# Kernel optimization log

Hardware: AMD Instinct MI355X
Metric: run time of the kernel (lower is better)

## Reference

```python
import jax, jax.numpy as jnp
import numpy as np

B, C, H, W, D = 4, 8, 160, 160, 160
N_PER = 100000
IMAGE_DIM = 160


def setup_inputs() -> dict:
    key = jax.random.key(0)
    k1, k2 = jax.random.split(key)
    image_features = jax.random.normal(k1, (B, C, H, W, D), dtype=jnp.float32)
    # coords uniform in [0, IMAGE_DIM); last 3 columns are x,y,z
    graph_features = jax.random.uniform(k2, (B * N_PER, 3), dtype=jnp.float32) * IMAGE_DIM
    batch = jnp.arange(B * N_PER, dtype=jnp.int32) // N_PER  # equal count per image (required by cat dim=0)
    return {
        "image_features": image_features,
        "graph_features": graph_features,
        "batch": batch,
        "image_dim": IMAGE_DIM,
    }


def _trilerp(image_features, graph_features, image_dim):
    Bn, Cc, Hh, Ww, Dd = image_features.shape
    n_per = graph_features.shape[0] // Bn
    dt = graph_features.dtype
    factor = jnp.asarray(image_dim, dt) / Hh  # original uses image_dim/h for all axes
    xyz = graph_features[:, -3:].reshape(Bn, n_per, 3) / factor  # [B, n, 3]
    x, y, z = xyz[..., 0], xyz[..., 1], xyz[..., 2]

    def bounds(v, size):
        lo = jnp.minimum(jnp.floor(v), size - 1)
        hi = jnp.minimum(jnp.ceil(v), size - 1)
        return lo, hi

    x1f, x2f = bounds(x, Hh)
    y1f, y2f = bounds(y, Ww)
    z1f, z2f = bounds(z, Dd)
    x1, x2 = x1f.astype(jnp.int32), x2f.astype(jnp.int32)
    y1, y2 = y1f.astype(jnp.int32), y2f.astype(jnp.int32)
    z1, z2 = z1f.astype(jnp.int32), z2f.astype(jnp.int32)
    # weights exactly as in original (degenerate-to-zero when floor==ceil, kept faithfully)
    wx, wx2 = x - x1f, x2f - x
    wy, wy2 = y - y1f, y2f - y
    wz, wz2 = z - z1f, z2f - z

    def per_image(img, x1, x2, y1, y2, z1, z2, wx, wx2, wy, wy2, wz, wz2):
        # img: [C, H, W, D]; indices/weights: [n]
        def g(xi, yi, zi):
            return img[:, xi, yi, zi]  # [C, n]

        def lerp_y(zc):
            lx1 = g(x2, y1, zc) * wx + g(x1, y1, zc) * wx2
            lx2 = g(x2, y2, zc) * wx + g(x1, y2, zc) * wx2
            return lx2 * wy + lx1 * wy2

        return lerp_y(z2) * wz + lerp_y(z1) * wz2  # [C, n]

    out = jax.vmap(per_image)(
        image_features, x1, x2, y1, y2, z1, z2, wx, wx2, wy, wy2, wz, wz2
    )  # [B, C, n]
    # torch.cat over batch along dim 0 of [C, n] blocks == reshape to [B*C, n]; then permute(1,0)
    return out.reshape(Bn * Cc, n_per).T  # [n, B*C]


def reference(image_features, graph_features, batch, image_dim):
    # batch is arange(N)//n_per (sorted, equal counts), so grouping == reshape; batch unused numerically
    return _trilerp(image_features, graph_features, image_dim)
```

## Files before the change

### kernel.cpp

```cpp
#include <hip/hip_runtime.h>

constexpr int B = 4, C = 8, H = 160, W = 160, Dd = 160, NPER = 100000;
constexpr long HWD = (long)H * W * Dd;
constexpr int  TOTAL_PTS = NPER * B;
constexpr int  TOTAL_OUT = NPER * B * C;
constexpr int  NKEYS = B * H * W;
constexpr int  SCAN_BLOCKS = NKEYS / 256;

typedef float f32x4 __attribute__((ext_vector_type(4)));

constexpr size_t WS_COUNTS_OFF = 0;
constexpr size_t WS_PART_OFF   = (size_t)NKEYS * 4;
constexpr size_t WS_PAY_OFF    = WS_PART_OFF + 4096;
constexpr size_t WS_NEEDED     = WS_PAY_OFF + (size_t)TOTAL_PTS * 16;

__device__ __forceinline__ float load_image_dim(const int* dimp) {
    int iv = dimp[0];
    return (iv > 0 && iv < 1000000) ? (float)iv : __int_as_float(iv);
}

struct Coord {
    int x1, x2, y1, y2, z1, z2;
    float wx, wx2, wy, wy2, wz, wz2;
};
__device__ __forceinline__ Coord coord_from_xyz(float gx, float gy, float gz,
                                                float factor) {
    Coord c;
    float x = gx / factor, y = gy / factor, z = gz / factor;
    float x1f = fminf(floorf(x), (float)(H - 1));
    float x2f = fminf(ceilf(x),  (float)(H - 1));
    float y1f = fminf(floorf(y), (float)(W - 1));
    float y2f = fminf(ceilf(y),  (float)(W - 1));
    float z1f = fminf(floorf(z), (float)(Dd - 1));
    float z2f = fminf(ceilf(z),  (float)(Dd - 1));
    c.x1 = max(0, (int)x1f); c.x2 = max(0, (int)x2f);
    c.y1 = max(0, (int)y1f); c.y2 = max(0, (int)y2f);
    c.z1 = max(0, (int)z1f); c.z2 = max(0, (int)z2f);
    c.wx = x - x1f; c.wx2 = x2f - x;
    c.wy = y - y1f; c.wy2 = y2f - y;
    c.wz = z - z1f; c.wz2 = z2f - z;
    return c;
}

__global__ __launch_bounds__(256) void zero_kernel(int* __restrict__ counts) {
    int i = blockIdx.x * 256 + threadIdx.x;
    if (i < NKEYS) counts[i] = 0;
}

__global__ __launch_bounds__(256) void hist_kernel(
    const float* __restrict__ gf, const int* __restrict__ dimp,
    int* __restrict__ counts)
{
    int p = blockIdx.x * 256 + threadIdx.x;
    if (p >= TOTAL_PTS) return;
    float factor = load_image_dim(dimp) / (float)H;
    int b = p / NPER;
    Coord c = coord_from_xyz(gf[(long)p*3], gf[(long)p*3+1], gf[(long)p*3+2], factor);
    atomicAdd(&counts[(b * H + c.x1) * W + c.y1], 1);
}

__global__ __launch_bounds__(256) void scanA_kernel(
    int* __restrict__ counts, int* __restrict__ partials)
{
    __shared__ int sm[256];
    int g = blockIdx.x * 256 + threadIdx.x;
    int v = counts[g];
    sm[threadIdx.x] = v;
    __syncthreads();
    for (int off = 1; off < 256; off <<= 1) {
        int t = (threadIdx.x >= off) ? sm[threadIdx.x - off] : 0;
        __syncthreads();
        sm[threadIdx.x] += t;
        __syncthreads();
    }
    counts[g] = sm[threadIdx.x] - v;
    if (threadIdx.x == 255) partials[blockIdx.x] = sm[255];
}

__global__ __launch_bounds__(512) void scanB_kernel(int* __restrict__ partials)
{
    __shared__ int sm[512];
    int t = threadIdx.x;
    int v = (t < SCAN_BLOCKS) ? partials[t] : 0;
    sm[t] = v;
    __syncthreads();
    for (int off = 1; off < 512; off <<= 1) {
        int u = (t >= off) ? sm[t - off] : 0;
        __syncthreads();
        sm[t] += u;
        __syncthreads();
    }
    if (t < SCAN_BLOCKS) partials[t] = sm[t] - v;
}

__global__ __launch_bounds__(256) void scanC_kernel(
    int* __restrict__ counts, const int* __restrict__ partials)
{
    int g = blockIdx.x * 256 + threadIdx.x;
    counts[g] += partials[blockIdx.x];
}

__global__ __launch_bounds__(256) void scatter_kernel(
    const float* __restrict__ gf, const int* __restrict__ dimp,
    int* __restrict__ counts, f32x4* __restrict__ payload)
{
    int p = blockIdx.x * 256 + threadIdx.x;
    if (p >= TOTAL_PTS) return;
    float factor = load_image_dim(dimp) / (float)H;
    int b = p / NPER;
    float gx = gf[(long)p*3], gy = gf[(long)p*3+1], gz = gf[(long)p*3+2];
    Coord c = coord_from_xyz(gx, gy, gz, factor);
    int pos = atomicAdd(&counts[(b * H + c.x1) * W + c.y1], 1);
    f32x4 rec;
    rec.x = __int_as_float(p); rec.y = gx; rec.z = gy; rec.w = gz;
    payload[pos] = rec;
}

__global__ __launch_bounds__(256) void gather_sorted(
    const float* __restrict__ img, const f32x4* __restrict__ payload,
    const int* __restrict__ dimp, float* __restrict__ out)
{
    int nwg = gridDim.x;
    int q = nwg >> 3, r = nwg & 7;
    int xcd = blockIdx.x & 7, idx = blockIdx.x >> 3;
    int wg = (xcd < r) ? xcd * (q + 1) + idx
                       : r * (q + 1) + (xcd - r) * q + idx;
    int t = wg * 256 + threadIdx.x;
    if (t >= TOTAL_OUT) return;
    int i = t >> 3, c = t & 7;

    f32x4 rec = payload[i];
    int p = __float_as_int(rec.x);
    int b = p / NPER;
    int j = p - b * NPER;

    float factor = load_image_dim(dimp) / (float)H;
    Coord cc = coord_from_xyz(rec.y, rec.z, rec.w, factor);

    const float* base = img + (long)(b * C + c) * HWD;
    const float* r11 = base + ((long)cc.x1 * W + cc.y1) * Dd;
    const float* r12 = base + ((long)cc.x1 * W + cc.y2) * Dd;
    const float* r21 = base + ((long)cc.x2 * W + cc.y1) * Dd;
    const float* r22 = base + ((long)cc.x2 * W + cc.y2) * Dd;

    float lx1_a = r21[cc.z2] * cc.wx + r11[cc.z2] * cc.wx2;
    float lx2_a = r22[cc.z2] * cc.wx + r12[cc.z2] * cc.wx2;
    float ly_a  = lx2_a * cc.wy + lx1_a * cc.wy2;
    float lx1_b = r21[cc.z1] * cc.wx + r11[cc.z1] * cc.wx2;
    float lx2_b = r22[cc.z1] * cc.wx + r12[cc.z1] * cc.wx2;
    float ly_b  = lx2_b * cc.wy + lx1_b * cc.wy2;
    float res = ly_a * cc.wz + ly_b * cc.wz2;

    __builtin_nontemporal_store(res, out + (long)j * 32 + b * 8 + c);
}

__global__ __launch_bounds__(256) void og_proj_direct(
    const float* __restrict__ img, const float* __restrict__ gf,
    const int* __restrict__ dimp, float* __restrict__ out)
{
    int o = blockIdx.x * 256 + threadIdx.x;
    if (o >= TOTAL_OUT) return;
    int j = o >> 5, bc = o & 31, b = bc >> 3, c = bc & 7;
    float factor = load_image_dim(dimp) / (float)H;
    long p = (long)b * NPER + j;
    Coord cc = coord_from_xyz(gf[p*3], gf[p*3+1], gf[p*3+2], factor);

    const float* base = img + (size_t)(b * C + c) * (size_t)HWD;
    size_t r11 = ((size_t)cc.x1 * W + cc.y1) * Dd;
    size_t r12 = ((size_t)cc.x1 * W + cc.y2) * Dd;
    size_t r21 = ((size_t)cc.x2 * W + cc.y1) * Dd;
    size_t r22 = ((size_t)cc.x2 * W + cc.y2) * Dd;

    float lx1_a = base[r21 + cc.z2] * cc.wx + base[r11 + cc.z2] * cc.wx2;
    float lx2_a = base[r22 + cc.z2] * cc.wx + base[r12 + cc.z2] * cc.wx2;
    float ly_a  = lx2_a * cc.wy + lx1_a * cc.wy2;
    float lx1_b = base[r21 + cc.z1] * cc.wx + base[r11 + cc.z1] * cc.wx2;
    float lx2_b = base[r22 + cc.z1] * cc.wx + base[r12 + cc.z1] * cc.wx2;
    float ly_b  = lx2_b * cc.wy + lx1_b * cc.wy2;
    out[o] = ly_a * cc.wz + ly_b * cc.wz2;
}

extern "C" void kernel_launch(void* const* d_in, const int* in_sizes, int n_in,
                              void* d_out, int out_size, void* d_ws, size_t ws_size,
                              hipStream_t stream) {
    const float* img  = (const float*)d_in[0];
    const float* gf   = (const float*)d_in[1];
    const int*   dimp = (const int*)d_in[3];
    float* out = (float*)d_out;

    if (ws_size >= WS_NEEDED) {
        int*   counts = (int*)((char*)d_ws + WS_COUNTS_OFF);
        int*   parts  = (int*)((char*)d_ws + WS_PART_OFF);
        f32x4* payld  = (f32x4*)((char*)d_ws + WS_PAY_OFF);

        int pblocks = (TOTAL_PTS + 255) / 256;
        zero_kernel<<<SCAN_BLOCKS, 256, 0, stream>>>(counts);
        hist_kernel<<<pblocks, 256, 0, stream>>>(gf, dimp, counts);
        scanA_kernel<<<SCAN_BLOCKS, 256, 0, stream>>>(counts, parts);
        scanB_kernel<<<1, 512, 0, stream>>>(parts);
        scanC_kernel<<<SCAN_BLOCKS, 256, 0, stream>>>(counts, parts);
        scatter_kernel<<<pblocks, 256, 0, stream>>>(gf, dimp, counts, payld);

        int gblocks = (TOTAL_OUT + 255) / 256;
        gather_sorted<<<gblocks, 256, 0, stream>>>(img, payld, dimp, out);
    } else {
        int blocks = (TOTAL_OUT + 255) / 256;
        og_proj_direct<<<blocks, 256, 0, stream>>>(img, gf, dimp, out);
    }
}
```

Baseline: 197.7 us.

## Bin points into 8x8 xy tiles and gather from LDS-staged image columns

Points are bucketed by coarse 8x8 (x,y) tiles instead of per-(x,y) column keys, which collapses the three-pass scan into a single-block scan. The gather kernel now runs one workgroup per tile. For each channel it stages the 9x9 haloed set of full z-columns into LDS, interpolates all of the tile's points from LDS, and writes each point's 8 channels as two vector stores. This replaces scattered global gathers with coalesced bulk loads. In exchange it streams roughly the whole image plus halo through LDS, and the synchronous load-then-compute steps have no overlap.

```diff
diff --git a/kernel.cpp b/kernel.cpp
--- a/kernel.cpp
+++ b/kernel.cpp
@@ -4,14 +4,18 @@
 constexpr long HWD = (long)H * W * Dd;
 constexpr int  TOTAL_PTS = NPER * B;
 constexpr int  TOTAL_OUT = NPER * B * C;
-constexpr int  NKEYS = B * H * W;
-constexpr int  SCAN_BLOCKS = NKEYS / 256;
+
+constexpr int  TS   = 8;
+constexpr int  TDIM = H / TS;
+constexpr int  NT   = B * TDIM * TDIM;
+constexpr int  HC   = TS + 1;
+constexpr int  ZV4  = Dd / 4;
 
 typedef float f32x4 __attribute__((ext_vector_type(4)));
 
-constexpr size_t WS_COUNTS_OFF = 0;
-constexpr size_t WS_PART_OFF   = (size_t)NKEYS * 4;
-constexpr size_t WS_PAY_OFF    = WS_PART_OFF + 4096;
+constexpr size_t WS_CURSOR_OFF = 0;
+constexpr size_t WS_OFFS_OFF   = 8192;
+constexpr size_t WS_PAY_OFF    = 16384;
 constexpr size_t WS_NEEDED     = WS_PAY_OFF + (size_t)TOTAL_PTS * 16;
 
 __device__ __forceinline__ float load_image_dim(const int* dimp) {
@@ -42,47 +46,42 @@
     return c;
 }
 
-__global__ __launch_bounds__(256) void zero_kernel(int* __restrict__ counts) {
+__device__ __forceinline__ int tile_key(int b, const Coord& c) {
+    return (b * TDIM + (c.x1 >> 3)) * TDIM + (c.y1 >> 3);
+}
+
+__global__ __launch_bounds__(256) void zero_kernel(int* __restrict__ cursor) {
     int i = blockIdx.x * 256 + threadIdx.x;
-    if (i < NKEYS) counts[i] = 0;
+    if (i < NT) cursor[i] = 0;
 }
 
 __global__ __launch_bounds__(256) void hist_kernel(
     const float* __restrict__ gf, const int* __restrict__ dimp,
-    int* __restrict__ counts)
+    int* __restrict__ cursor)
 {
     int p = blockIdx.x * 256 + threadIdx.x;
     if (p >= TOTAL_PTS) return;
     float factor = load_image_dim(dimp) / (float)H;
     int b = p / NPER;
     Coord c = coord_from_xyz(gf[(long)p*3], gf[(long)p*3+1], gf[(long)p*3+2], factor);
-    atomicAdd(&counts[(b * H + c.x1) * W + c.y1], 1);
-}
-
-__global__ __launch_bounds__(256) void scanA_kernel(
-    int* __restrict__ counts, int* __restrict__ partials)
-{
-    __shared__ int sm[256];
-    int g = blockIdx.x * 256 + threadIdx.x;
-    int v = counts[g];
-    sm[threadIdx.x] = v;
-    __syncthreads();
-    for (int off = 1; off < 256; off <<= 1) {
-        int t = (threadIdx.x >= off) ? sm[threadIdx.x - off] : 0;
-        __syncthreads();
-        sm[threadIdx.x] += t;
-        __syncthreads();
-    }
-    counts[g] = sm[threadIdx.x] - v;
-    if (threadIdx.x == 255) partials[blockIdx.x] = sm[255];
-}
-
-__global__ __launch_bounds__(512) void scanB_kernel(int* __restrict__ partials)
-{
+    atomicAdd(&cursor[tile_key(b, c)], 1);
+}
+
+__global__ __launch_bounds__(512) void scan_kernel(
+    int* __restrict__ cursor, int* __restrict__ offsets)
+{
+    constexpr int CH = (NT + 511) / 512;
     __shared__ int sm[512];
     int t = threadIdx.x;
-    int v = (t < SCAN_BLOCKS) ? partials[t] : 0;
-    sm[t] = v;
+    int loc[CH];
+    int s = 0;
+    #pragma unroll
+    for (int k = 0; k < CH; ++k) {
+        int g = t * CH + k;
+        int v = (g < NT) ? cursor[g] : 0;
+        loc[k] = v; s += v;
+    }
+    sm[t] = s;
     __syncthreads();
     for (int off = 1; off < 512; off <<= 1) {
         int u = (t >= off) ? sm[t - off] : 0;
@@ -90,19 +89,18 @@
         sm[t] += u;
         __syncthreads();
     }
-    if (t < SCAN_BLOCKS) partials[t] = sm[t] - v;
-}
-
-__global__ __launch_bounds__(256) void scanC_kernel(
-    int* __restrict__ counts, const int* __restrict__ partials)
-{
-    int g = blockIdx.x * 256 + threadIdx.x;
-    counts[g] += partials[blockIdx.x];
+    int run = sm[t] - s;
+    #pragma unroll
+    for (int k = 0; k < CH; ++k) {
+        int g = t * CH + k;
+        if (g < NT) { offsets[g] = run; cursor[g] = run; run += loc[k]; }
+    }
+    if (t == 511) offsets[NT] = sm[511];
 }
 
 __global__ __launch_bounds__(256) void scatter_kernel(
     const float* __restrict__ gf, const int* __restrict__ dimp,
-    int* __restrict__ counts, f32x4* __restrict__ payload)
+    int* __restrict__ cursor, f32x4* __restrict__ payload)
 {
     int p = blockIdx.x * 256 + threadIdx.x;
     if (p >= TOTAL_PTS) return;
@@ -110,48 +108,85 @@
     int b = p / NPER;
     float gx = gf[(long)p*3], gy = gf[(long)p*3+1], gz = gf[(long)p*3+2];
     Coord c = coord_from_xyz(gx, gy, gz, factor);
-    int pos = atomicAdd(&counts[(b * H + c.x1) * W + c.y1], 1);
+    int pos = atomicAdd(&cursor[tile_key(b, c)], 1);
     f32x4 rec;
     rec.x = __int_as_float(p); rec.y = gx; rec.z = gy; rec.w = gz;
     payload[pos] = rec;
 }
 
-__global__ __launch_bounds__(256) void gather_sorted(
+__global__ __launch_bounds__(512) void gather_tiled(
     const float* __restrict__ img, const f32x4* __restrict__ payload,
-    const int* __restrict__ dimp, float* __restrict__ out)
+    const int* __restrict__ offsets, const int* __restrict__ dimp,
+    float* __restrict__ out)
 {
     int nwg = gridDim.x;
     int q = nwg >> 3, r = nwg & 7;
     int xcd = blockIdx.x & 7, idx = blockIdx.x >> 3;
-    int wg = (xcd < r) ? xcd * (q + 1) + idx
-                       : r * (q + 1) + (xcd - r) * q + idx;
-    int t = wg * 256 + threadIdx.x;
-    if (t >= TOTAL_OUT) return;
-    int i = t >> 3, c = t & 7;
-
-    f32x4 rec = payload[i];
-    int p = __float_as_int(rec.x);
-    int b = p / NPER;
-    int j = p - b * NPER;
-
-    float factor = load_image_dim(dimp) / (float)H;
-    Coord cc = coord_from_xyz(rec.y, rec.z, rec.w, factor);
-
-    const float* base = img + (long)(b * C + c) * HWD;
-    const float* r11 = base + ((long)cc.x1 * W + cc.y1) * Dd;
-    const float* r12 = base + ((long)cc.x1 * W + cc.y2) * Dd;
-    const float* r21 = base + ((long)cc.x2 * W + cc.y1) * Dd;
-    const float* r22 = base + ((long)cc.x2 * W + cc.y2) * Dd;
-
-    float lx1_a = r21[cc.z2] * cc.wx + r11[cc.z2] * cc.wx2;
-    float lx2_a = r22[cc.z2] * cc.wx + r12[cc.z2] * cc.wx2;
-    float ly_a  = lx2_a * cc.wy + lx1_a * cc.wy2;
-    float lx1_b = r21[cc.z1] * cc.wx + r11[cc.z1] * cc.wx2;
-    float lx2_b = r22[cc.z1] * cc.wx + r12[cc.z1] * cc.wx2;
-    float ly_b  = lx2_b * cc.wy + lx1_b * cc.wy2;
-    float res = ly_a * cc.wz + ly_b * cc.wz2;
-
-    __builtin_nontemporal_store(res, out + (long)j * 32 + b * 8 + c);
+    int tile = (xcd < r) ? xcd * (q + 1) + idx
+                         : r * (q + 1) + (xcd - r) * q + idx;
+
+    int ty = tile % TDIM;
+    int tx = (tile / TDIM) % TDIM;
+    int b  = tile / (TDIM * TDIM);
+    int beg = offsets[tile], end = offsets[tile + 1];
+    int npts = end - beg;
+    if (npts == 0) return;
+
+    int x0 = tx * TS, y0 = ty * TS;
+    __shared__ float lds[HC * HC * Dd];
+
+    float factor = load_image_dim(dimp) / (float)H;
+    int tid = threadIdx.x;
+
+    for (int cb = 0; cb < npts; cb += 512) {
+        int i = cb + tid;
+        bool act = i < npts;
+        f32x4 rec;
+        rec.x = 0.f; rec.y = 0.f; rec.z = 0.f; rec.w = 0.f;
+        if (act) rec = payload[beg + i];
+
+        Coord cc = coord_from_xyz(rec.y, rec.z, rec.w, factor);
+        int i11 = ((cc.x1 - x0) * HC + (cc.y1 - y0)) * Dd;
+        int i12 = ((cc.x1 - x0) * HC + (cc.y2 - y0)) * Dd;
+        int i21 = ((cc.x2 - x0) * HC + (cc.y1 - y0)) * Dd;
+        int i22 = ((cc.x2 - x0) * HC + (cc.y2 - y0)) * Dd;
+
+        float res[8];
+        #pragma unroll
+        for (int c = 0; c < 8; ++c) {
+            __syncthreads();
+            const float* chbase = img + (long)(b * C + c) * HWD;
+            for (int l = tid; l < HC * HC * ZV4; l += 512) {
+                int col = l / ZV4, qq = l - col * ZV4;
+                int cx = col / HC, cy = col - cx * HC;
+                int x = min(x0 + cx, H - 1), y = min(y0 + cy, W - 1);
+                const f32x4* src = reinterpret_cast<const f32x4*>(
+                    chbase + ((long)x * W + y) * Dd) + qq;
+                *reinterpret_cast<f32x4*>(&lds[col * Dd + qq * 4]) = *src;
+            }
+            __syncthreads();
+            if (act) {
+                float lx1_a = lds[i21 + cc.z2] * cc.wx + lds[i11 + cc.z2] * cc.wx2;
+                float lx2_a = lds[i22 + cc.z2] * cc.wx + lds[i12 + cc.z2] * cc.wx2;
+                float ly_a  = lx2_a * cc.wy + lx1_a * cc.wy2;
+                float lx1_b = lds[i21 + cc.z1] * cc.wx + lds[i11 + cc.z1] * cc.wx2;
+                float lx2_b = lds[i22 + cc.z1] * cc.wx + lds[i12 + cc.z1] * cc.wx2;
+                float ly_b  = lx2_b * cc.wy + lx1_b * cc.wy2;
+                res[c] = ly_a * cc.wz + ly_b * cc.wz2;
+            }
+        }
+
+        if (act) {
+            int p = __float_as_int(rec.x);
+            int j = p - b * NPER;
+            f32x4 r0, r1;
+            r0[0] = res[0]; r0[1] = res[1]; r0[2] = res[2]; r0[3] = res[3];
+            r1[0] = res[4]; r1[1] = res[5]; r1[2] = res[6]; r1[3] = res[7];
+            float* dst = out + (long)j * 32 + b * 8;
+            __builtin_nontemporal_store(r0, reinterpret_cast<f32x4*>(dst));
+            __builtin_nontemporal_store(r1, reinterpret_cast<f32x4*>(dst + 4));
+        }
+    }
 }
 
 __global__ __launch_bounds__(256) void og_proj_direct(
@@ -189,20 +224,16 @@
     float* out = (float*)d_out;
 
     if (ws_size >= WS_NEEDED) {
-        int*   counts = (int*)((char*)d_ws + WS_COUNTS_OFF);
-        int*   parts  = (int*)((char*)d_ws + WS_PART_OFF);
-        f32x4* payld  = (f32x4*)((char*)d_ws + WS_PAY_OFF);
+        int*   cursor  = (int*)((char*)d_ws + WS_CURSOR_OFF);
+        int*   offsets = (int*)((char*)d_ws + WS_OFFS_OFF);
+        f32x4* payld   = (f32x4*)((char*)d_ws + WS_PAY_OFF);
 
         int pblocks = (TOTAL_PTS + 255) / 256;
-        zero_kernel<<<SCAN_BLOCKS, 256, 0, stream>>>(counts);
-        hist_kernel<<<pblocks, 256, 0, stream>>>(gf, dimp, counts);
-        scanA_kernel<<<SCAN_BLOCKS, 256, 0, stream>>>(counts, parts);
-        scanB_kernel<<<1, 512, 0, stream>>>(parts);
-        scanC_kernel<<<SCAN_BLOCKS, 256, 0, stream>>>(counts, parts);
-        scatter_kernel<<<pblocks, 256, 0, stream>>>(gf, dimp, counts, payld);
-
-        int gblocks = (TOTAL_OUT + 255) / 256;
-        gather_sorted<<<gblocks, 256, 0, stream>>>(img, payld, dimp, out);
+        zero_kernel<<<(NT + 255) / 256, 256, 0, stream>>>(cursor);
+        hist_kernel<<<pblocks, 256, 0, stream>>>(gf, dimp, cursor);
+        scan_kernel<<<1, 512, 0, stream>>>(cursor, offsets);
+        scatter_kernel<<<pblocks, 256, 0, stream>>>(gf, dimp, cursor, payld);
+        gather_tiled<<<NT, 512, 0, stream>>>(img, payld, offsets, dimp, out);
     } else {
         int blocks = (TOTAL_OUT + 255) / 256;
         og_proj_direct<<<blocks, 256, 0, stream>>>(img, gf, dimp, out);
```

New measurement: 252.9 us. 27.9% more time.
